# Optimization experiments

Measured on AMD Instinct MI355X. Metric: run time of the kernel, lower is better.

The kernel has to match this reference:

```python
import jax, jax.numpy as jnp
import numpy as np


def setup_inputs() -> dict:
    key = jax.random.key(0)
    k1, k2, k3 = jax.random.split(key, 3)
    B, C, H, W = 32, 128, 64, 64
    z = jax.random.normal(k1, (B, C, H, W, 2), dtype=jnp.float32)
    gamma = jnp.eye(2, dtype=jnp.float32) / jnp.sqrt(jnp.float32(2.0)) \
        + 0.01 * jax.random.normal(k2, (2, 2), dtype=jnp.float32)
    beta = 0.01 * jax.random.normal(k3, (2,), dtype=jnp.float32)
    return {"z": z, "gamma": gamma, "beta": beta}


def reference(z, gamma, beta):
    # z: [B, C, H, W, 2] real view of complex input. Training-mode C_BatchNorm.
    B, C, H, W, _ = z.shape
    N = C * H * W
    zf = z.reshape(B, N, 2)
    mu = jnp.mean(zf, axis=0)                 # [N, 2]
    xc = zf - mu                              # [B, N, 2]
    # Per-position 2x2 covariance over batch (unbiased, /(B-1)).
    sigma = jnp.einsum('bni,bnj->nij', xc, xc) / jnp.asarray(B - 1, zf.dtype)  # [N,2,2]
    # Closed-form 2x2 "inverse-sqrt" as written in the source: (M + s*I)/t.
    trace = sigma[:, 0, 0] + sigma[:, 1, 1]
    det = sigma[:, 0, 0] * sigma[:, 1, 1] - sigma[:, 0, 1] * sigma[:, 1, 0]
    s = jnp.sqrt(det)
    t = jnp.sqrt(trace + 2.0 * s)
    eye2 = jnp.eye(2, dtype=zf.dtype)
    m_inv = (sigma + s[:, None, None] * eye2) / t[:, None, None]  # [N,2,2]
    # Whitening (per-position 2x2 matvec) + affine gamma/beta.
    o = jnp.einsum('nij,bnj->bni', m_inv, xc)                     # [B,N,2]
    o = jnp.einsum('ij,bnj->bni', gamma, o) + beta                # [B,N,2]
    return o.reshape(B, C, H, W, 2)
```

## Files before the change

### kernel.cpp

```cpp
#include <hip/hip_runtime.h>


constexpr int BATCH = 32;

__global__ __launch_bounds__(256) void cbn_kernel(
    const float* __restrict__ z,
    const float* __restrict__ gamma,
    const float* __restrict__ beta,
    float* __restrict__ out,
    int N)
{
    int n = blockIdx.x * blockDim.x + threadIdx.x;
    if (n >= N) return;

    const float2* __restrict__ zp = (const float2*)z;
    float2* __restrict__ op = (float2*)out;

    float2 v[BATCH];
#pragma unroll
    for (int b = 0; b < BATCH; ++b) {
        v[b] = zp[(size_t)b * N + n];
    }

    float mx = 0.f, my = 0.f;
#pragma unroll
    for (int b = 0; b < BATCH; ++b) { mx += v[b].x; my += v[b].y; }
    mx *= (1.0f / BATCH);
    my *= (1.0f / BATCH);

    float sxx = 0.f, sxy = 0.f, syy = 0.f;
#pragma unroll
    for (int b = 0; b < BATCH; ++b) {
        float dx = v[b].x - mx;
        float dy = v[b].y - my;
        sxx += dx * dx;
        sxy += dx * dy;
        syy += dy * dy;
    }
    const float inv = 1.0f / (BATCH - 1);
    sxx *= inv; sxy *= inv; syy *= inv;

    float trace = sxx + syy;
    float det = sxx * syy - sxy * sxy;
    float s = sqrtf(det);
    float t = sqrtf(trace + 2.0f * s);
    float rt = 1.0f / t;

    float a00 = (sxx + s) * rt;
    float a01 = sxy * rt;
    float a11 = (syy + s) * rt;

    float g00 = gamma[0], g01 = gamma[1], g10 = gamma[2], g11 = gamma[3];
    float b0 = beta[0], b1 = beta[1];

    float c00 = g00 * a00 + g01 * a01;
    float c01 = g00 * a01 + g01 * a11;
    float c10 = g10 * a00 + g11 * a01;
    float c11 = g10 * a01 + g11 * a11;

#pragma unroll
    for (int b = 0; b < BATCH; ++b) {
        float dx = v[b].x - mx;
        float dy = v[b].y - my;
        float2 o;
        o.x = c00 * dx + c01 * dy + b0;
        o.y = c10 * dx + c11 * dy + b1;
        op[(size_t)b * N + n] = o;
    }
}

extern "C" void kernel_launch(void* const* d_in, const int* in_sizes, int n_in,
                              void* d_out, int out_size, void* d_ws, size_t ws_size,
                              hipStream_t stream) {
    const float* z     = (const float*)d_in[0];
    const float* gamma = (const float*)d_in[1];
    const float* beta  = (const float*)d_in[2];
    float* out = (float*)d_out;

    int N = in_sizes[0] / (BATCH * 2);

    dim3 block(256);
    dim3 grid((N + block.x - 1) / block.x);
    hipLaunchKernelGGL(cbn_kernel, grid, block, 0, stream, z, gamma, beta, out, N);
}
```

Baseline: 48.13 us.

## Process two positions per thread with float4 loads and one-pass moments

Each thread now handles two adjacent positions and uses 16-byte float4 loads and stores instead of 8-byte float2. Covariance is built in one pass from raw sums and sums of squares, so the 32 batch values no longer need to stay in registers. The input is then read a second time for the output pass, relying on cache hits. This cuts register pressure and raises occupancy, at the cost of re-reading input and the weaker numerical stability of the E[x^2]-mu^2 formula.

```diff
diff --git a/kernel.cpp b/kernel.cpp
--- a/kernel.cpp
+++ b/kernel.cpp
@@ -4,82 +4,85 @@
 constexpr int BATCH = 32;
 
 __global__ __launch_bounds__(256) void cbn_kernel(
-    const float* __restrict__ z,
+    const float4* __restrict__ z,
     const float* __restrict__ gamma,
     const float* __restrict__ beta,
-    float* __restrict__ out,
-    int N)
+    float4* __restrict__ out,
+    int N2)
 {
-    int n = blockIdx.x * blockDim.x + threadIdx.x;
-    if (n >= N) return;
+    int i = blockIdx.x * blockDim.x + threadIdx.x;
+    if (i >= N2) return;
 
-    const float2* __restrict__ zp = (const float2*)z;
-    float2* __restrict__ op = (float2*)out;
-
-    float2 v[BATCH];
+    float sx0 = 0.f, sy0 = 0.f, sxx0 = 0.f, sxy0 = 0.f, syy0 = 0.f;
+    float sx1 = 0.f, sy1 = 0.f, sxx1 = 0.f, sxy1 = 0.f, syy1 = 0.f;
 #pragma unroll
     for (int b = 0; b < BATCH; ++b) {
-        v[b] = zp[(size_t)b * N + n];
+        float4 v = z[(size_t)b * N2 + i];
+        sx0 += v.x; sy0 += v.y;
+        sxx0 = fmaf(v.x, v.x, sxx0);
+        sxy0 = fmaf(v.x, v.y, sxy0);
+        syy0 = fmaf(v.y, v.y, syy0);
+        sx1 += v.z; sy1 += v.w;
+        sxx1 = fmaf(v.z, v.z, sxx1);
+        sxy1 = fmaf(v.z, v.w, sxy1);
+        syy1 = fmaf(v.w, v.w, syy1);
     }
 
-    float mx = 0.f, my = 0.f;
-#pragma unroll
-    for (int b = 0; b < BATCH; ++b) { mx += v[b].x; my += v[b].y; }
-    mx *= (1.0f / BATCH);
-    my *= (1.0f / BATCH);
-
-    float sxx = 0.f, sxy = 0.f, syy = 0.f;
-#pragma unroll
-    for (int b = 0; b < BATCH; ++b) {
-        float dx = v[b].x - mx;
-        float dy = v[b].y - my;
-        sxx += dx * dx;
-        sxy += dx * dy;
-        syy += dy * dy;
-    }
-    const float inv = 1.0f / (BATCH - 1);
-    sxx *= inv; sxy *= inv; syy *= inv;
-
-    float trace = sxx + syy;
-    float det = sxx * syy - sxy * sxy;
-    float s = sqrtf(det);
-    float t = sqrtf(trace + 2.0f * s);
-    float rt = 1.0f / t;
-
-    float a00 = (sxx + s) * rt;
-    float a01 = sxy * rt;
-    float a11 = (syy + s) * rt;
+    const float invB  = 1.0f / BATCH;
+    const float invB1 = 1.0f / (BATCH - 1);
 
     float g00 = gamma[0], g01 = gamma[1], g10 = gamma[2], g11 = gamma[3];
-    float b0 = beta[0], b1 = beta[1];
+    float be0 = beta[0], be1 = beta[1];
 
-    float c00 = g00 * a00 + g01 * a01;
-    float c01 = g00 * a01 + g01 * a11;
-    float c10 = g10 * a00 + g11 * a01;
-    float c11 = g10 * a01 + g11 * a11;
+    float mx0 = sx0 * invB, my0 = sy0 * invB;
+    float cxx0 = (sxx0 - BATCH * mx0 * mx0) * invB1;
+    float cxy0 = (sxy0 - BATCH * mx0 * my0) * invB1;
+    float cyy0 = (syy0 - BATCH * my0 * my0) * invB1;
+    float s0 = sqrtf(cxx0 * cyy0 - cxy0 * cxy0);
+    float rt0 = 1.0f / sqrtf(cxx0 + cyy0 + 2.0f * s0);
+    float a00_0 = (cxx0 + s0) * rt0, a01_0 = cxy0 * rt0, a11_0 = (cyy0 + s0) * rt0;
+    float c00_0 = g00 * a00_0 + g01 * a01_0;
+    float c01_0 = g00 * a01_0 + g01 * a11_0;
+    float c10_0 = g10 * a00_0 + g11 * a01_0;
+    float c11_0 = g10 * a01_0 + g11 * a11_0;
+
+    float mx1 = sx1 * invB, my1 = sy1 * invB;
+    float cxx1 = (sxx1 - BATCH * mx1 * mx1) * invB1;
+    float cxy1 = (sxy1 - BATCH * mx1 * my1) * invB1;
+    float cyy1 = (syy1 - BATCH * my1 * my1) * invB1;
+    float s1 = sqrtf(cxx1 * cyy1 - cxy1 * cxy1);
+    float rt1 = 1.0f / sqrtf(cxx1 + cyy1 + 2.0f * s1);
+    float a00_1 = (cxx1 + s1) * rt1, a01_1 = cxy1 * rt1, a11_1 = (cyy1 + s1) * rt1;
+    float c00_1 = g00 * a00_1 + g01 * a01_1;
+    float c01_1 = g00 * a01_1 + g01 * a11_1;
+    float c10_1 = g10 * a00_1 + g11 * a01_1;
+    float c11_1 = g10 * a01_1 + g11 * a11_1;
 
 #pragma unroll
     for (int b = 0; b < BATCH; ++b) {
-        float dx = v[b].x - mx;
-        float dy = v[b].y - my;
-        float2 o;
-        o.x = c00 * dx + c01 * dy + b0;
-        o.y = c10 * dx + c11 * dy + b1;
-        op[(size_t)b * N + n] = o;
+        float4 v = z[(size_t)b * N2 + i];
+        float dx0 = v.x - mx0, dy0 = v.y - my0;
+        float dx1 = v.z - mx1, dy1 = v.w - my1;
+        float4 o;
+        o.x = fmaf(c00_0, dx0, fmaf(c01_0, dy0, be0));
+        o.y = fmaf(c10_0, dx0, fmaf(c11_0, dy0, be1));
+        o.z = fmaf(c00_1, dx1, fmaf(c01_1, dy1, be0));
+        o.w = fmaf(c10_1, dx1, fmaf(c11_1, dy1, be1));
+        out[(size_t)b * N2 + i] = o;
     }
 }
 
 extern "C" void kernel_launch(void* const* d_in, const int* in_sizes, int n_in,
                               void* d_out, int out_size, void* d_ws, size_t ws_size,
                               hipStream_t stream) {
-    const float* z     = (const float*)d_in[0];
+    const float4* z    = (const float4*)d_in[0];
     const float* gamma = (const float*)d_in[1];
     const float* beta  = (const float*)d_in[2];
-    float* out = (float*)d_out;
+    float4* out = (float4*)d_out;
 
-    int N = in_sizes[0] / (BATCH * 2);
+    int N2 = in_sizes[0] / (BATCH * 4);
 
     dim3 block(256);
-    dim3 grid((N + block.x - 1) / block.x);
-    hipLaunchKernelGGL(cbn_kernel, grid, block, 0, stream, z, gamma, beta, out, N);
+    dim3 grid((N2 + block.x - 1) / block.x);
+    hipLaunchKernelGGL(cbn_kernel, grid, block, 0, stream, z, gamma, beta, out, N2);
 }
```

After: 70.25 us. 46.0% more time.
